# Optimization experiments

Hardware: AMD Instinct MI355X
Metric: run time of the kernel (lower is better)

The kernel has to match this reference:

```python
import jax, jax.numpy as jnp
import numpy as np

B, T, V, H = 512, 1024, 27, 512  # batch, seq, N+1 vocab, hidden


def setup_inputs() -> dict:
    key = jax.random.key(0)
    ks = jax.random.split(key, 7)
    s_ih = 1.0 / np.sqrt(H)
    return {
        "x": jax.random.uniform(ks[0], (B, T, V), dtype=jnp.float32),
        "W_ih": jax.random.normal(ks[1], (3 * H, V), dtype=jnp.float32) * s_ih,
        "W_hh": jax.random.normal(ks[2], (3 * H, H), dtype=jnp.float32) * s_ih,
        "b_ih": jax.random.normal(ks[3], (3 * H,), dtype=jnp.float32) * s_ih,
        "b_hh": jax.random.normal(ks[4], (3 * H,), dtype=jnp.float32) * s_ih,
        "W_dec": jax.random.normal(ks[5], (V, H), dtype=jnp.float32) * s_ih,
        "b_dec": jax.random.normal(ks[6], (V,), dtype=jnp.float32) * s_ih,
    }


def reference(x, W_ih, W_hh, b_ih, b_hh, W_dec, b_dec):
    # x: (B, T, V). Precompute the input projection for all timesteps at once.
    gi_all = jnp.einsum("btv,gv->btg", x, W_ih) + b_ih  # (B, T, 3H)
    h0 = jnp.zeros((x.shape[0], W_hh.shape[1]), dtype=x.dtype)

    def step(h, gi_t):
        gh = h @ W_hh.T + b_hh                       # (B, 3H)
        i_r, i_z, i_n = jnp.split(gi_t, 3, axis=-1)
        h_r, h_z, h_n = jnp.split(gh, 3, axis=-1)
        r = jax.nn.sigmoid(i_r + h_r)
        z = jax.nn.sigmoid(i_z + h_z)
        n = jnp.tanh(i_n + r * h_n)
        h_new = (1.0 - z) * n + z * h                # torch GRUCell update
        return h_new, h_new

    _, hs = jax.lax.scan(step, h0, jnp.swapaxes(gi_all, 0, 1))  # hs: (T, B, H)
    hs = jnp.swapaxes(hs, 0, 1)                                  # (B, T, H)
    logits = jnp.einsum("bth,vh->btv", hs, W_dec) + b_dec        # per-step decode
    return logits
```

## Files before the change

kernel.cpp:

```cpp
#include <hip/hip_runtime.h>
#include <math.h>

#define Bsz 512
#define Tsz 1024
#define Vsz 27
#define Hsz 512
#define BH (Bsz * Hsz)
#define TV (Tsz * Vsz)
#define NBLK 256
#define NT 512
#define BT 64
#define JB 32
#define NG 48

typedef float f32x4 __attribute__((ext_vector_type(4)));
typedef short s16x8 __attribute__((ext_vector_type(8)));
typedef unsigned int u32x4 __attribute__((ext_vector_type(4)));
#define MFMA __builtin_amdgcn_mfma_f32_16x16x32_bf16

#define WS_CNT  ((size_t)2 * 3 * BH * 2)
#define WS_FLG  (WS_CNT + 4096)
#define WS_DSTG (WS_FLG + 32768)
#define WS_WXG  (WS_DSTG + (size_t)2 * 16 * 512 * 2)

__device__ __forceinline__ unsigned short btrunc(float x) {
    return (unsigned short)(__float_as_uint(x) >> 16);
}
__device__ __forceinline__ float bup(unsigned short b) {
    return __uint_as_float(((unsigned)b) << 16);
}
__device__ __forceinline__ unsigned short brne(float x) {
    unsigned u = __float_as_uint(x);
    return (unsigned short)((u + 0x7FFFu + ((u >> 16) & 1u)) >> 16);
}
__device__ __forceinline__ __amdgpu_buffer_rsrc_t make_rsrc(void* p, unsigned bytes) {
    return __builtin_amdgcn_make_buffer_rsrc(p, (short)0, (int)bytes, 0x00020000);
}
template<bool FAST>
__device__ __forceinline__ s16x8 loadA(__amdgpu_buffer_rsrc_t r, int off) {
    u32x4 d = __builtin_amdgcn_raw_buffer_load_b128(r, off, 0, FAST ? 0 : 0x11);
    return __builtin_bit_cast(s16x8, d);
}
template<bool FAST>
__device__ __forceinline__ void storeH(__amdgpu_buffer_rsrc_t r, int off, unsigned short v) {
    __builtin_amdgcn_raw_buffer_store_b16(v, r, off, 0, FAST ? 0 : 0x11);
}
__device__ __forceinline__ unsigned flag_get(unsigned* p) {
    return __hip_atomic_load(p, __ATOMIC_RELAXED, __HIP_MEMORY_SCOPE_AGENT);
}
__device__ __forceinline__ void gate_spin(unsigned* flags, int bt, int c, int step) {
    unsigned* fA = flags + (size_t)((bt << 5) + (c << 1)) * 32;
    unsigned* fB = fA + 32;
    while ((int)flag_get(fA) < step || (int)flag_get(fB) < step)
        __builtin_amdgcn_s_sleep(2);
}

#define PROD6(ACC, B1_, B2_, B3_, A1_, A2_, A3_) do { \
    ACC = MFMA(A1_, B1_, ACC, 0, 0, 0); \
    ACC = MFMA(A1_, B2_, ACC, 0, 0, 0); \
    ACC = MFMA(A2_, B1_, ACC, 0, 0, 0); \
    ACC = MFMA(A1_, B3_, ACC, 0, 0, 0); \
    ACC = MFMA(A2_, B2_, ACC, 0, 0, 0); \
    ACC = MFMA(A3_, B1_, ACC, 0, 0, 0); } while (0)
#define PROD5(ACC, B1_, B2_, A1_, A2_, A3_) do { \
    ACC = MFMA(A1_, B1_, ACC, 0, 0, 0); \
    ACC = MFMA(A1_, B2_, ACC, 0, 0, 0); \
    ACC = MFMA(A2_, B1_, ACC, 0, 0, 0); \
    ACC = MFMA(A2_, B2_, ACC, 0, 0, 0); \
    ACC = MFMA(A3_, B1_, ACC, 0, 0, 0); } while (0)

__global__ void init_ws_kernel(unsigned short* __restrict__ hpl, unsigned* __restrict__ cntr,
                               unsigned short* __restrict__ Dstg, unsigned short* __restrict__ Wxg,
                               const float* __restrict__ W_ih, const float* __restrict__ W_dec)
{
    size_t gid = (size_t)blockIdx.x * 256 + threadIdx.x;
    size_t gsz = (size_t)gridDim.x * 256;
    for (size_t i = gid; i < (size_t)(2 * 3 * BH * 2) / 16; i += gsz)
        ((uint4*)hpl)[i] = make_uint4(0u, 0u, 0u, 0u);
    for (size_t i = gid; i < 9216; i += gsz) cntr[i] = 0u;
    for (size_t i = gid; i < 2 * 16 * 512; i += gsz) {
        int e = i & 7, ln2 = (i >> 3) & 63, c = (i >> 9) & 15, jj = (int)(i >> 13);
        int cc2 = ln2 & 15, qq2 = ln2 >> 4;
        int k = c * 32 + qq2 * 8 + e;
        int vr = jj * 16 + cc2;
        Dstg[i] = (vr < Vsz) ? brne(W_dec[(size_t)vr * Hsz + k]) : (unsigned short)0;
    }
    for (size_t i = gid; i < 1536 * 64; i += gsz) {
        int k = i & 31, p = (i >> 5) & 1, grow = (int)(i >> 6);
        float v = (k < Vsz) ? W_ih[grow * Vsz + k] : 0.f;
        unsigned short t1 = btrunc(v); float r1 = v - bup(t1);
        unsigned short t2 = btrunc(r1);
        Wxg[i] = p ? t2 : t1;
    }
}

__device__ __forceinline__ void group_barrier(unsigned* c, unsigned target) {
    __syncthreads();
    if (threadIdx.x == 0) {
        __hip_atomic_fetch_add(c, 1u, __ATOMIC_RELAXED, __HIP_MEMORY_SCOPE_AGENT);
        while (__hip_atomic_load(c, __ATOMIC_RELAXED, __HIP_MEMORY_SCOPE_AGENT) < target)
            __builtin_amdgcn_s_sleep(2);
    }
    __syncthreads();
}

template<bool FAST>
__device__ __forceinline__ void gru_loop(
    const float* __restrict__ x, float* __restrict__ out,
    const unsigned short* __restrict__ Dstg, const unsigned short* __restrict__ Wxg,
    unsigned* __restrict__ flags, __amdgpu_buffer_rsrc_t hrs,
    const unsigned short* Bst, float* xs, float* nscr,
    const float* bihL, const float* bhhL, float bdv,
    int tid, int bt, int j, int b0, int g0)
{
    const int w = tid >> 6, ln = tid & 63;
    const int m = w & 3, half = w >> 2;
    const int cc = ln & 15, qq = ln >> 4;
    const int rowA = (m << 4) + cc;
    const int xr = tid >> 3, xc = (tid & 7) << 2;
    const int vcol = (j << 4) + cc;
    const int rowBase = ((b0 + rowA) * Hsz + (qq << 3)) << 1;
    unsigned* myflag = flags + (size_t)((bt << 5) + j) * 32;

    float hk[4] = {0.f, 0.f, 0.f, 0.f};

    for (int i = 0; i <= Tsz; ++i) {
        if (FAST) asm volatile("buffer_inv" ::: "memory");
        float xreg[4];
        if (i + 1 < Tsz) {
            #pragma unroll
            for (int e = 0; e < 4; ++e) {
                int ci = xc + e;
                xreg[e] = (ci < Vsz) ? x[(size_t)(b0 + xr) * TV + (size_t)(i + 1) * Vsz + ci] : 0.f;
            }
        }
        const int voffA0 = (i & 1) * (3 * BH * 2) + rowBase;

        f32x4 accR = {0,0,0,0}, accZ = {0,0,0,0}, accNi = {0,0,0,0};
        f32x4 accNh = {0,0,0,0}, accD = {0,0,0,0};

        gate_spin(flags, bt, 0, i);
        s16x8 A1c = loadA<FAST>(hrs, voffA0);
        s16x8 A2c = loadA<FAST>(hrs, voffA0 + BH * 2);
        s16x8 A3c = loadA<FAST>(hrs, voffA0 + 2 * BH * 2);
        unsigned fA1 = flag_get(flags + (size_t)((bt << 5) + 2) * 32);
        unsigned fB1 = flag_get(flags + (size_t)((bt << 5) + 3) * 32);
        #pragma unroll
        for (int c = 0; c < 16; ++c) {
            s16x8 A1n, A2n, A3n;
            if (c < 15) {
                const int cn = c + 1;
                if ((int)fA1 < i || (int)fB1 < i) gate_spin(flags, bt, cn, i);
                A1n = loadA<FAST>(hrs, voffA0 + cn * 64);
                A2n = loadA<FAST>(hrs, voffA0 + cn * 64 + BH * 2);
                A3n = loadA<FAST>(hrs, voffA0 + cn * 64 + 2 * BH * 2);
                if (c < 14) {
                    const int c2 = c + 2;
                    fA1 = flag_get(flags + (size_t)((bt << 5) + (c2 << 1)) * 32);
                    fB1 = flag_get(flags + (size_t)((bt << 5) + (c2 << 1) + 1) * 32);
                }
            }
            const unsigned short* bs = Bst + (size_t)(c * 9) * 512 + (ln << 3);
            if (half == 0) {
                s16x8 B1 = *(const s16x8*)(bs);
                s16x8 B2 = *(const s16x8*)(bs + 512);
                s16x8 B3 = *(const s16x8*)(bs + 1024);
                PROD6(accR, B1, B2, B3, A1c, A2c, A3c);
                s16x8 C1 = *(const s16x8*)(bs + 1536);
                s16x8 C2 = *(const s16x8*)(bs + 2048);
                s16x8 C3 = *(const s16x8*)(bs + 2560);
                PROD6(accZ, C1, C2, C3, A1c, A2c, A3c);
            } else {
                s16x8 N1 = *(const s16x8*)(bs + 3072);
                s16x8 N2 = *(const s16x8*)(bs + 3584);
                s16x8 N3 = *(const s16x8*)(bs + 4096);
                PROD6(accNh, N1, N2, N3, A1c, A2c, A3c);
                if (j < 2) {
                    s16x8 D1 = *(const s16x8*)(Dstg + (size_t)((j << 4) + c) * 512 + (ln << 3));
                    accD = MFMA(A1c, D1, accD, 0, 0, 0);
                    accD = MFMA(A2c, D1, accD, 0, 0, 0);
                }
            }
            A1c = A1n; A2c = A2n; A3c = A3n;
        }

        if (half == 0 && i < Tsz) {
            s16x8 A1, A2, A3;
            #pragma unroll
            for (int e = 0; e < 8; ++e) {
                float v = xs[rowA * 32 + (qq << 3) + e];
                unsigned short s1 = btrunc(v); float r1 = v - bup(s1);
                unsigned short s2 = btrunc(r1); float r2 = r1 - bup(s2);
                unsigned short s3 = btrunc(r2);
                A1[e] = (short)s1; A2[e] = (short)s2; A3[e] = (short)s3;
            }
            {
                const unsigned short* wb = Wxg + (size_t)(g0 + cc) * 64 + (qq << 3);
                s16x8 B1 = *(const s16x8*)(wb);
                s16x8 B2 = *(const s16x8*)(wb + 32);
                PROD5(accR, B1, B2, A1, A2, A3);
            }
            {
                const unsigned short* wb = Wxg + (size_t)(Hsz + g0 + cc) * 64 + (qq << 3);
                s16x8 B1 = *(const s16x8*)(wb);
                s16x8 B2 = *(const s16x8*)(wb + 32);
                PROD5(accZ, B1, B2, A1, A2, A3);
            }
            {
                const unsigned short* wb = Wxg + (size_t)(2 * Hsz + g0 + cc) * 64 + (qq << 3);
                s16x8 B1 = *(const s16x8*)(wb);
                s16x8 B2 = *(const s16x8*)(wb + 32);
                PROD5(accNi, B1, B2, A1, A2, A3);
            }
        }

        __syncthreads();
        if (half == 1 && i < Tsz)
            *(f32x4*)&nscr[(size_t)(m * 64 + ln) * 4] = accNh;
        if (i + 1 < Tsz) {
            #pragma unroll
            for (int e = 0; e < 4; ++e) xs[xr * 32 + xc + e] = xreg[e];
        }
        __syncthreads();

        if (half == 0 && i < Tsz) {
            const int wpar = ((i + 1) & 1) * (3 * BH * 2);
            const float* nh4 = &nscr[(size_t)(m * 64 + ln) * 4];
            #pragma unroll
            for (int r = 0; r < 4; ++r) {
                float rv = accR[r] + bihL[cc] + bhhL[cc];
                float zv = accZ[r] + bihL[16 + cc] + bhhL[16 + cc];
                float ni = accNi[r] + bihL[32 + cc];
                float nh = nh4[r] + bhhL[32 + cc];
                float rg = 1.f / (1.f + expf(-rv));
                float zg = 1.f / (1.f + expf(-zv));
                float ng = tanhf(ni + rg * nh);
                float hv = (1.f - zg) * ng + zg * hk[r];
                hk[r] = hv;
                int e2 = wpar + (((b0 + (m << 4) + (qq << 2) + r) * Hsz + g0 + cc) << 1);
                unsigned short s1 = btrunc(hv); float r1 = hv - bup(s1);
                unsigned short s2 = btrunc(r1); float r2 = r1 - bup(s2);
                unsigned short s3 = btrunc(r2);
                storeH<FAST>(hrs, e2, s1);
                storeH<FAST>(hrs, e2 + BH * 2, s2);
                storeH<FAST>(hrs, e2 + 2 * BH * 2, s3);
            }
        }
        if (i < Tsz) {
            asm volatile("s_waitcnt vmcnt(0)" ::: "memory");
            __syncthreads();
            if (tid == 0)
                __hip_atomic_store(myflag, (unsigned)(i + 1), __ATOMIC_RELAXED,
                                   __HIP_MEMORY_SCOPE_AGENT);
        }
        if (i > 0 && half == 1 && j < 2 && vcol < Vsz) {
            #pragma unroll
            for (int r = 0; r < 4; ++r) {
                size_t brow = (size_t)(b0 + (m << 4) + (qq << 2) + r);
                out[brow * TV + (size_t)(i - 1) * Vsz + vcol] = accD[r] + bdv;
            }
        }
    }
}

__global__ __launch_bounds__(NT, 2) void gru_persist(
    const float* __restrict__ x, const float* __restrict__ W_ih,
    const float* __restrict__ W_hh, const float* __restrict__ b_ih,
    const float* __restrict__ b_hh, const float* __restrict__ W_dec,
    const float* __restrict__ b_dec, char* __restrict__ wsb,
    float* __restrict__ out)
{
    __shared__ unsigned short Bst[16 * 9 * 512];
    __shared__ float xs[BT * 32];
    __shared__ float nscr[4 * 64 * 4];
    __shared__ float bihL[NG], bhhL[NG];
    __shared__ int fastFlag;

    unsigned short* hpl = (unsigned short*)wsb;
    unsigned* cbase = (unsigned*)(wsb + WS_CNT);
    unsigned* flags = (unsigned*)(wsb + WS_FLG);
    unsigned short* Dstg = (unsigned short*)(wsb + WS_DSTG);
    unsigned short* Wxg  = (unsigned short*)(wsb + WS_WXG);

    const int tid = threadIdx.x;
    const int bt  = blockIdx.x & 7;
    const int j   = blockIdx.x >> 3;
    const int b0  = bt * BT;
    const int g0  = j * 16;
    unsigned* pcnt  = cbase + 16 + bt;
    unsigned* xmask = cbase + 32 + bt;

    for (int idx = tid; idx < 16 * 9 * 512; idx += NT) {
        int e = idx & 7, ln2 = (idx >> 3) & 63, s = idx >> 9;
        int p = s % 3, t = (s / 3) % 3, c = s / 9;
        int cc2 = ln2 & 15, qq2 = ln2 >> 4;
        int k = c * 32 + qq2 * 8 + e;
        int grow = t * Hsz + g0 + cc2;
        float v = W_hh[(size_t)grow * Hsz + k];
        unsigned short t1 = btrunc(v); float r1 = v - bup(t1);
        unsigned short t2 = btrunc(r1); float r2 = r1 - bup(t2);
        unsigned short t3 = btrunc(r2);
        Bst[idx] = (p == 0) ? t1 : (p == 1) ? t2 : t3;
    }
    if (tid < NG) {
        int grow = (tid >> 4) * Hsz + g0 + (tid & 15);
        bihL[tid] = b_ih[grow]; bhhL[tid] = b_hh[grow];
    }
    {
        int xr = tid >> 3, xc = (tid & 7) << 2;
        #pragma unroll
        for (int e = 0; e < 4; ++e) {
            int ci = xc + e;
            xs[xr * 32 + ci] = (ci < Vsz) ? x[(size_t)(b0 + xr) * TV + ci] : 0.f;
        }
    }
    if (tid == 0) {
        unsigned xcc;
        asm volatile("s_getreg_b32 %0, hwreg(20, 0, 32)" : "=s"(xcc));
        __hip_atomic_fetch_or(xmask, 1u << (xcc & 31), __ATOMIC_RELAXED,
                              __HIP_MEMORY_SCOPE_AGENT);
        asm volatile("s_waitcnt vmcnt(0)" ::: "memory");
    }
    group_barrier(pcnt, JB);
    if (tid == 0) {
        unsigned f = __hip_atomic_load(xmask, __ATOMIC_RELAXED, __HIP_MEMORY_SCOPE_AGENT);
        fastFlag = (__popc(f) == 1) ? 1 : 0;
    }
    __syncthreads();
    const bool fastv = (fastFlag != 0);

    const int cc = tid & 15;
    const int vcol = (j << 4) + cc;
    const float bdv = (j < 2 && vcol < Vsz) ? b_dec[vcol] : 0.f;
    __amdgpu_buffer_rsrc_t hrs = make_rsrc((void*)hpl, (unsigned)(2u * 3u * BH * 2u));

    if (fastv)
        gru_loop<true>(x, out, Dstg, Wxg, flags, hrs, Bst, xs, nscr, bihL, bhhL, bdv,
                       tid, bt, j, b0, g0);
    else
        gru_loop<false>(x, out, Dstg, Wxg, flags, hrs, Bst, xs, nscr, bihL, bhhL, bdv,
                        tid, bt, j, b0, g0);
}

extern "C" void kernel_launch(void* const* d_in, const int* in_sizes, int n_in,
                              void* d_out, int out_size, void* d_ws, size_t ws_size,
                              hipStream_t stream) {
    const float* x     = (const float*)d_in[0];
    const float* W_ih  = (const float*)d_in[1];
    const float* W_hh  = (const float*)d_in[2];
    const float* b_ih  = (const float*)d_in[3];
    const float* b_hh  = (const float*)d_in[4];
    const float* W_dec = (const float*)d_in[5];
    const float* b_dec = (const float*)d_in[6];
    float* out = (float*)d_out;
    char* wsb  = (char*)d_ws;

    init_ws_kernel<<<768, 256, 0, stream>>>(
        (unsigned short*)wsb, (unsigned*)(wsb + WS_CNT),
        (unsigned short*)(wsb + WS_DSTG), (unsigned short*)(wsb + WS_WXG),
        W_ih, W_dec);

    gru_persist<<<dim3(NBLK), dim3(NT), 0, stream>>>(
        x, W_ih, W_hh, b_ih, b_hh, W_dec, b_dec, wsb, out);
}
```

Baseline: 14.59 ms.

## Give each wave its own 8 batch rows with per-wave flags, dropping block barriers

Each of the 8 waves now owns 8 batch rows and computes all three gates plus the decoder for them, instead of pairing waves to split the gate work through shared memory. Readiness flags become per-wave (bt, m, j), so waves wait on the specific producer waves they depend on, and the per-step __syncthreads, the LDS scratch for x and the n-gate, and the shared bias arrays are removed. The h-state loads now prefetch two chunks ahead through a three-slot ring. The cost is redundant MFMA work: only the lanes with qq<2 carry useful rows, so half of each 16-row tile is duplicated, and there are more flags to poll.

```diff
diff --git a/kernel.cpp b/kernel.cpp
--- a/kernel.cpp
+++ b/kernel.cpp
@@ -9,9 +9,7 @@
 #define TV (Tsz * Vsz)
 #define NBLK 256
 #define NT 512
-#define BT 64
 #define JB 32
-#define NG 48
 
 typedef float f32x4 __attribute__((ext_vector_type(4)));
 typedef short s16x8 __attribute__((ext_vector_type(8)));
@@ -20,7 +18,7 @@
 
 #define WS_CNT  ((size_t)2 * 3 * BH * 2)
 #define WS_FLG  (WS_CNT + 4096)
-#define WS_DSTG (WS_FLG + 32768)
+#define WS_DSTG (WS_FLG + 262144)
 #define WS_WXG  (WS_DSTG + (size_t)2 * 16 * 512 * 2)
 
 __device__ __forceinline__ unsigned short btrunc(float x) {
@@ -45,11 +43,14 @@
 __device__ __forceinline__ void storeH(__amdgpu_buffer_rsrc_t r, int off, unsigned short v) {
     __builtin_amdgcn_raw_buffer_store_b16(v, r, off, 0, FAST ? 0 : 0x11);
 }
+__device__ __forceinline__ unsigned* flag_ptr(unsigned* flags, int bt, int m, int jp) {
+    return flags + (size_t)((((bt << 3) + m) << 5) + jp) * 32;
+}
 __device__ __forceinline__ unsigned flag_get(unsigned* p) {
     return __hip_atomic_load(p, __ATOMIC_RELAXED, __HIP_MEMORY_SCOPE_AGENT);
 }
-__device__ __forceinline__ void gate_spin(unsigned* flags, int bt, int c, int step) {
-    unsigned* fA = flags + (size_t)((bt << 5) + (c << 1)) * 32;
+__device__ __forceinline__ void gate2(unsigned* flags, int bt, int m, int c, int step) {
+    unsigned* fA = flag_ptr(flags, bt, m, c << 1);
     unsigned* fB = fA + 32;
     while ((int)flag_get(fA) < step || (int)flag_get(fB) < step)
         __builtin_amdgcn_s_sleep(2);
@@ -77,7 +78,7 @@
     size_t gsz = (size_t)gridDim.x * 256;
     for (size_t i = gid; i < (size_t)(2 * 3 * BH * 2) / 16; i += gsz)
         ((uint4*)hpl)[i] = make_uint4(0u, 0u, 0u, 0u);
-    for (size_t i = gid; i < 9216; i += gsz) cntr[i] = 0u;
+    for (size_t i = gid; i < 66560; i += gsz) cntr[i] = 0u;
     for (size_t i = gid; i < 2 * 16 * 512; i += gsz) {
         int e = i & 7, ln2 = (i >> 3) & 63, c = (i >> 9) & 15, jj = (int)(i >> 13);
         int cc2 = ln2 & 15, qq2 = ln2 >> 4;
@@ -109,86 +110,93 @@
     const float* __restrict__ x, float* __restrict__ out,
     const unsigned short* __restrict__ Dstg, const unsigned short* __restrict__ Wxg,
     unsigned* __restrict__ flags, __amdgpu_buffer_rsrc_t hrs,
-    const unsigned short* Bst, float* xs, float* nscr,
-    const float* bihL, const float* bhhL, float bdv,
+    const unsigned short* Bst,
+    float bih_r, float bih_z, float bih_n,
+    float bhh_r, float bhh_z, float bhh_n, float bdv,
     int tid, int bt, int j, int b0, int g0)
 {
     const int w = tid >> 6, ln = tid & 63;
-    const int m = w & 3, half = w >> 2;
+    const int m = w;
     const int cc = ln & 15, qq = ln >> 4;
-    const int rowA = (m << 4) + cc;
-    const int xr = tid >> 3, xc = (tid & 7) << 2;
+    const int arow = b0 + (m << 3) + (cc & 7);
+    const int rowBase = (arow * Hsz + (qq << 3)) << 1;
+    unsigned* myflag = flag_ptr(flags, bt, m, j);
     const int vcol = (j << 4) + cc;
-    const int rowBase = ((b0 + rowA) * Hsz + (qq << 3)) << 1;
-    unsigned* myflag = flags + (size_t)((bt << 5) + j) * 32;
 
     float hk[4] = {0.f, 0.f, 0.f, 0.f};
 
     for (int i = 0; i <= Tsz; ++i) {
         if (FAST) asm volatile("buffer_inv" ::: "memory");
-        float xreg[4];
-        if (i + 1 < Tsz) {
+        float xreg[8];
+        if (i < Tsz) {
             #pragma unroll
-            for (int e = 0; e < 4; ++e) {
-                int ci = xc + e;
-                xreg[e] = (ci < Vsz) ? x[(size_t)(b0 + xr) * TV + (size_t)(i + 1) * Vsz + ci] : 0.f;
+            for (int e = 0; e < 8; ++e) {
+                int k = (qq << 3) + e;
+                xreg[e] = (k < Vsz) ? x[(size_t)arow * TV + (size_t)i * Vsz + k] : 0.f;
             }
         }
         const int voffA0 = (i & 1) * (3 * BH * 2) + rowBase;
 
-        f32x4 accR = {0,0,0,0}, accZ = {0,0,0,0}, accNi = {0,0,0,0};
-        f32x4 accNh = {0,0,0,0}, accD = {0,0,0,0};
-
-        gate_spin(flags, bt, 0, i);
-        s16x8 A1c = loadA<FAST>(hrs, voffA0);
-        s16x8 A2c = loadA<FAST>(hrs, voffA0 + BH * 2);
-        s16x8 A3c = loadA<FAST>(hrs, voffA0 + 2 * BH * 2);
-        unsigned fA1 = flag_get(flags + (size_t)((bt << 5) + 2) * 32);
-        unsigned fB1 = flag_get(flags + (size_t)((bt << 5) + 3) * 32);
+        f32x4 accR = {0,0,0,0}, accZ = {0,0,0,0}, accNh = {0,0,0,0};
+        f32x4 accNi = {0,0,0,0}, accD = {0,0,0,0};
+
+        s16x8 A1s[3], A2s[3], A3s[3];
+        gate2(flags, bt, m, 0, i);
+        A1s[0] = loadA<FAST>(hrs, voffA0);
+        A2s[0] = loadA<FAST>(hrs, voffA0 + BH * 2);
+        A3s[0] = loadA<FAST>(hrs, voffA0 + 2 * BH * 2);
+        gate2(flags, bt, m, 1, i);
+        A1s[1] = loadA<FAST>(hrs, voffA0 + 64);
+        A2s[1] = loadA<FAST>(hrs, voffA0 + 64 + BH * 2);
+        A3s[1] = loadA<FAST>(hrs, voffA0 + 64 + 2 * BH * 2);
+        unsigned pfa = flag_get(flag_ptr(flags, bt, m, 4));
+        unsigned pfb = flag_get(flag_ptr(flags, bt, m, 5));
         #pragma unroll
         for (int c = 0; c < 16; ++c) {
-            s16x8 A1n, A2n, A3n;
-            if (c < 15) {
-                const int cn = c + 1;
-                if ((int)fA1 < i || (int)fB1 < i) gate_spin(flags, bt, cn, i);
-                A1n = loadA<FAST>(hrs, voffA0 + cn * 64);
-                A2n = loadA<FAST>(hrs, voffA0 + cn * 64 + BH * 2);
-                A3n = loadA<FAST>(hrs, voffA0 + cn * 64 + 2 * BH * 2);
-                if (c < 14) {
-                    const int c2 = c + 2;
-                    fA1 = flag_get(flags + (size_t)((bt << 5) + (c2 << 1)) * 32);
-                    fB1 = flag_get(flags + (size_t)((bt << 5) + (c2 << 1) + 1) * 32);
+            if (c + 2 < 16) {
+                if ((int)pfa < i || (int)pfb < i) gate2(flags, bt, m, c + 2, i);
+                const int s2 = (c + 2) % 3;
+                A1s[s2] = loadA<FAST>(hrs, voffA0 + (c + 2) * 64);
+                A2s[s2] = loadA<FAST>(hrs, voffA0 + (c + 2) * 64 + BH * 2);
+                A3s[s2] = loadA<FAST>(hrs, voffA0 + (c + 2) * 64 + 2 * BH * 2);
+                if (c + 3 < 16) {
+                    pfa = flag_get(flag_ptr(flags, bt, m, (c + 3) << 1));
+                    pfb = flag_get(flag_ptr(flags, bt, m, ((c + 3) << 1) + 1));
                 }
             }
+            const int sl = c % 3;
+            s16x8 A1 = A1s[sl], A2 = A2s[sl], A3 = A3s[sl];
             const unsigned short* bs = Bst + (size_t)(c * 9) * 512 + (ln << 3);
-            if (half == 0) {
+            {
                 s16x8 B1 = *(const s16x8*)(bs);
                 s16x8 B2 = *(const s16x8*)(bs + 512);
                 s16x8 B3 = *(const s16x8*)(bs + 1024);
-                PROD6(accR, B1, B2, B3, A1c, A2c, A3c);
+                PROD6(accR, B1, B2, B3, A1, A2, A3);
+            }
+            {
                 s16x8 C1 = *(const s16x8*)(bs + 1536);
                 s16x8 C2 = *(const s16x8*)(bs + 2048);
                 s16x8 C3 = *(const s16x8*)(bs + 2560);
-                PROD6(accZ, C1, C2, C3, A1c, A2c, A3c);
-            } else {
+                PROD6(accZ, C1, C2, C3, A1, A2, A3);
+            }
+            {
                 s16x8 N1 = *(const s16x8*)(bs + 3072);
                 s16x8 N2 = *(const s16x8*)(bs + 3584);
                 s16x8 N3 = *(const s16x8*)(bs + 4096);
-                PROD6(accNh, N1, N2, N3, A1c, A2c, A3c);
-                if (j < 2) {
-                    s16x8 D1 = *(const s16x8*)(Dstg + (size_t)((j << 4) + c) * 512 + (ln << 3));
-                    accD = MFMA(A1c, D1, accD, 0, 0, 0);
-                    accD = MFMA(A2c, D1, accD, 0, 0, 0);
-                }
-            }
-            A1c = A1n; A2c = A2n; A3c = A3n;
-        }
-
-        if (half == 0 && i < Tsz) {
+                PROD6(accNh, N1, N2, N3, A1, A2, A3);
+            }
+            if (j < 2) {
+                s16x8 D1 = *(const s16x8*)(Dstg + (size_t)((j << 4) + c) * 512 + (ln << 3));
+                accD = MFMA(A1, D1, accD, 0, 0, 0);
+                accD = MFMA(A2, D1, accD, 0, 0, 0);
+            }
+        }
+
+        if (i < Tsz) {
             s16x8 A1, A2, A3;
             #pragma unroll
             for (int e = 0; e < 8; ++e) {
-                float v = xs[rowA * 32 + (qq << 3) + e];
+                float v = xreg[e];
                 unsigned short s1 = btrunc(v); float r1 = v - bup(s1);
                 unsigned short s2 = btrunc(r1); float r2 = r1 - bup(s2);
                 unsigned short s3 = btrunc(r2);
@@ -214,30 +222,21 @@
             }
         }
 
-        __syncthreads();
-        if (half == 1 && i < Tsz)
-            *(f32x4*)&nscr[(size_t)(m * 64 + ln) * 4] = accNh;
-        if (i + 1 < Tsz) {
-            #pragma unroll
-            for (int e = 0; e < 4; ++e) xs[xr * 32 + xc + e] = xreg[e];
-        }
-        __syncthreads();
-
-        if (half == 0 && i < Tsz) {
+        if (i < Tsz && qq < 2) {
             const int wpar = ((i + 1) & 1) * (3 * BH * 2);
-            const float* nh4 = &nscr[(size_t)(m * 64 + ln) * 4];
             #pragma unroll
             for (int r = 0; r < 4; ++r) {
-                float rv = accR[r] + bihL[cc] + bhhL[cc];
-                float zv = accZ[r] + bihL[16 + cc] + bhhL[16 + cc];
-                float ni = accNi[r] + bihL[32 + cc];
-                float nh = nh4[r] + bhhL[32 + cc];
+                float rv = accR[r] + bih_r + bhh_r;
+                float zv = accZ[r] + bih_z + bhh_z;
+                float nh = accNh[r] + bhh_n;
+                float ni = accNi[r] + bih_n;
                 float rg = 1.f / (1.f + expf(-rv));
                 float zg = 1.f / (1.f + expf(-zv));
                 float ng = tanhf(ni + rg * nh);
                 float hv = (1.f - zg) * ng + zg * hk[r];
                 hk[r] = hv;
-                int e2 = wpar + (((b0 + (m << 4) + (qq << 2) + r) * Hsz + g0 + cc) << 1);
+                int brow = b0 + (m << 3) + (qq << 2) + r;
+                int e2 = wpar + ((brow * Hsz + g0 + cc) << 1);
                 unsigned short s1 = btrunc(hv); float r1 = hv - bup(s1);
                 unsigned short s2 = btrunc(r1); float r2 = r1 - bup(s2);
                 unsigned short s3 = btrunc(r2);
@@ -248,15 +247,14 @@
         }
         if (i < Tsz) {
             asm volatile("s_waitcnt vmcnt(0)" ::: "memory");
-            __syncthreads();
-            if (tid == 0)
+            if (ln == 0)
                 __hip_atomic_store(myflag, (unsigned)(i + 1), __ATOMIC_RELAXED,
                                    __HIP_MEMORY_SCOPE_AGENT);
         }
-        if (i > 0 && half == 1 && j < 2 && vcol < Vsz) {
+        if (i > 0 && j < 2 && qq < 2 && vcol < Vsz) {
             #pragma unroll
             for (int r = 0; r < 4; ++r) {
-                size_t brow = (size_t)(b0 + (m << 4) + (qq << 2) + r);
+                size_t brow = (size_t)(b0 + (m << 3) + (qq << 2) + r);
                 out[brow * TV + (size_t)(i - 1) * Vsz + vcol] = accD[r] + bdv;
             }
         }
@@ -271,9 +269,6 @@
     float* __restrict__ out)
 {
     __shared__ unsigned short Bst[16 * 9 * 512];
-    __shared__ float xs[BT * 32];
-    __shared__ float nscr[4 * 64 * 4];
-    __shared__ float bihL[NG], bhhL[NG];
     __shared__ int fastFlag;
 
     unsigned short* hpl = (unsigned short*)wsb;
@@ -285,7 +280,7 @@
     const int tid = threadIdx.x;
     const int bt  = blockIdx.x & 7;
     const int j   = blockIdx.x >> 3;
-    const int b0  = bt * BT;
+    const int b0  = bt * 64;
     const int g0  = j * 16;
     unsigned* pcnt  = cbase + 16 + bt;
     unsigned* xmask = cbase + 32 + bt;
@@ -302,18 +297,6 @@
         unsigned short t3 = btrunc(r2);
         Bst[idx] = (p == 0) ? t1 : (p == 1) ? t2 : t3;
     }
-    if (tid < NG) {
-        int grow = (tid >> 4) * Hsz + g0 + (tid & 15);
-        bihL[tid] = b_ih[grow]; bhhL[tid] = b_hh[grow];
-    }
-    {
-        int xr = tid >> 3, xc = (tid & 7) << 2;
-        #pragma unroll
-        for (int e = 0; e < 4; ++e) {
-            int ci = xc + e;
-            xs[xr * 32 + ci] = (ci < Vsz) ? x[(size_t)(b0 + xr) * TV + ci] : 0.f;
-        }
-    }
     if (tid == 0) {
         unsigned xcc;
         asm volatile("s_getreg_b32 %0, hwreg(20, 0, 32)" : "=s"(xcc));
@@ -330,15 +313,23 @@
     const bool fastv = (fastFlag != 0);
 
     const int cc = tid & 15;
+    const float bih_r = b_ih[g0 + cc];
+    const float bih_z = b_ih[Hsz + g0 + cc];
+    const float bih_n = b_ih[2 * Hsz + g0 + cc];
+    const float bhh_r = b_hh[g0 + cc];
+    const float bhh_z = b_hh[Hsz + g0 + cc];
+    const float bhh_n = b_hh[2 * Hsz + g0 + cc];
     const int vcol = (j << 4) + cc;
     const float bdv = (j < 2 && vcol < Vsz) ? b_dec[vcol] : 0.f;
     __amdgpu_buffer_rsrc_t hrs = make_rsrc((void*)hpl, (unsigned)(2u * 3u * BH * 2u));
 
     if (fastv)
-        gru_loop<true>(x, out, Dstg, Wxg, flags, hrs, Bst, xs, nscr, bihL, bhhL, bdv,
+        gru_loop<true>(x, out, Dstg, Wxg, flags, hrs, Bst,
+                       bih_r, bih_z, bih_n, bhh_r, bhh_z, bhh_n, bdv,
                        tid, bt, j, b0, g0);
     else
-        gru_loop<false>(x, out, Dstg, Wxg, flags, hrs, Bst, xs, nscr, bihL, bhhL, bdv,
+        gru_loop<false>(x, out, Dstg, Wxg, flags, hrs, Bst,
+                        bih_r, bih_z, bih_n, bhh_r, bhh_z, bhh_n, bdv,
                         tid, bt, j, b0, g0);
 }
 
```

After: 15.52 ms. +6.4%, slower.
